# Kernel optimization log

Measured on AMD Instinct MI355X. Metric: run time of the kernel, lower is better.

## Reference

```python
import jax, jax.numpy as jnp
import numpy as np


def setup_inputs() -> dict:
    key = jax.random.key(0)
    k0, k1, k2, k3, k4 = jax.random.split(key, 5)
    B, d_inner, L, d_state = 64, 384, 197, 16
    x = jax.random.normal(k0, (B, d_inner, L), dtype=jnp.float32)
    # deltaA = exp(delta*A) lies in (0,1); uniform keeps the recurrence stable
    deltaA = jax.random.uniform(k1, (B, d_inner, L, d_state), dtype=jnp.float32)
    deltaB = jax.random.normal(k2, (B, d_inner, L, d_state), dtype=jnp.float32)
    C = jax.random.normal(k3, (B, d_state, L), dtype=jnp.float32)
    D = jax.random.normal(k4, (d_inner,), dtype=jnp.float32)
    return {"x": x, "deltaA": deltaA, "deltaB": deltaB, "C": C, "D": D}


def reference(x, deltaA, deltaB, C, D):
    """Selective scan: h_t = deltaB_t*x_t + deltaA_t*h_{t-1}; y_t = h_t @ C_t.
    x:(B,d,L) deltaA/deltaB:(B,d,L,n) C:(B,n,L) D:(d,)
    """
    deltaB_x = deltaB * x[..., None]              # (B,d,L,n)
    dA_t = jnp.moveaxis(deltaA, 2, 0)             # (L,B,d,n)
    dBx_t = jnp.moveaxis(deltaB_x, 2, 0)          # (L,B,d,n)
    C_t = jnp.moveaxis(C, 2, 0)                   # (L,B,n)

    def step(h, inputs):
        a, bx, c = inputs
        h = bx + a * h                            # (B,d,n)
        y = jnp.einsum("bdn,bn->bd", h, c)        # (B,d)
        return h, y

    h0 = jnp.zeros(dA_t.shape[1:], dtype=x.dtype)
    _, ys = jax.lax.scan(step, h0, (dA_t, dBx_t, C_t))  # ys: (L,B,d)
    y = jnp.moveaxis(ys, 0, 2)                    # (B,d,L)
    return y + x * D[:, None]
```

## Files before the change

### kernel.cpp

```cpp
#include <hip/hip_runtime.h>


#define B_   64
#define DIN  384
#define L_   197
#define N_   16
#define BUFW 2176
#define WAVEW (2*BUFW)
#define CS_OFF (2*WAVEW)
#define LDSW (CS_OFF + L_*N_)

typedef unsigned int u32as1 __attribute__((address_space(1)));
typedef unsigned int u32as3 __attribute__((address_space(3)));

__device__ __forceinline__ void gll16(const float* g, float* l) {
    __builtin_amdgcn_global_load_lds((const u32as1*)g, (u32as3*)l, 16, 0, 0);
}
__device__ __forceinline__ void gll4(const float* g, float* l) {
    __builtin_amdgcn_global_load_lds((const u32as1*)g, (u32as3*)l, 4, 0, 0);
}

template<int CTRL>
__device__ __forceinline__ float dppadd(float p) {
    return p + __int_as_float(__builtin_amdgcn_update_dpp(
        0, __float_as_int(p), CTRL, 0xF, 0xF, true));
}
__device__ __forceinline__ float sum16(float p) {
    p = dppadd<0xB1>(p);
    p = dppadd<0x4E>(p);
    p = dppadd<0x141>(p);
    p = dppadd<0x140>(p);
    return p;
}

__global__ __launch_bounds__(128)
void ssm_burst(const float* __restrict__ x, const float* __restrict__ dA,
               const float* __restrict__ dB, const float* __restrict__ C,
               const float* __restrict__ D, float* __restrict__ y)
{
    __shared__ __align__(16) float lds[LDSW];

    const int tid = threadIdx.x;
    const int b   = blockIdx.y;
    const int d0  = blockIdx.x * 8;

    const float* Cg = C + (size_t)b * (N_ * L_);
    for (int i = tid; i < N_ * L_; i += 128) {
        const int n = i / L_;
        const int t = i - n * L_;
        lds[CS_OFF + t * N_ + n] = Cg[i];
    }
    __syncthreads();

    const int wav  = tid >> 6;
    const int lane = tid & 63;
    const int g    = lane >> 4;
    const int n    = lane & 15;

    const int bd0 = b * DIN + d0 + wav * 4;
    const float* Arow = dA + (size_t)bd0 * (L_ * N_);
    const float* Brow = dB + (size_t)bd0 * (L_ * N_);
    const float* Xrow = x  + (size_t)bd0 * L_;
    float*       Yrow = y  + (size_t)(bd0 + g) * L_;
    const float  Dd   = D[d0 + wav * 4 + g];

    float* wl = lds + wav * WAVEW;
    const int lane4 = lane * 4;

#define STAGE(buf, t0) do { \
    float* _d = wl + (buf) * BUFW; \
    gll16(Arow + 0*(L_*N_) + (t0)*16 + lane4, _d + 0*264); \
    gll16(Arow + 1*(L_*N_) + (t0)*16 + lane4, _d + 1*264); \
    gll16(Arow + 2*(L_*N_) + (t0)*16 + lane4, _d + 2*264); \
    gll16(Arow + 3*(L_*N_) + (t0)*16 + lane4, _d + 3*264); \
    gll16(Brow + 0*(L_*N_) + (t0)*16 + lane4, _d + 1056 + 0*264); \
    gll16(Brow + 1*(L_*N_) + (t0)*16 + lane4, _d + 1056 + 1*264); \
    gll16(Brow + 2*(L_*N_) + (t0)*16 + lane4, _d + 1056 + 2*264); \
    gll16(Brow + 3*(L_*N_) + (t0)*16 + lane4, _d + 1056 + 3*264); \
    gll4(Xrow + g * L_ + (t0) + n, _d + 2112); \
} while (0)

#define STEP(j, xv, tg0, J0) do { \
    if ((j) >= (J0)) { \
        const float _a = _ab[g*264 + (j)*16 + n]; \
        const float _g = _ab[1056 + g*264 + (j)*16 + n]; \
        h = fmaf(_a, h, _g * (xv)); \
        float _p = h * lds[CS_OFF + ((tg0)+(j))*16 + n]; \
        _p = sum16(_p); \
        const float _yt = fmaf((xv), Dd, _p); \
        _ys = (n == (j)) ? _yt : _ys; \
    } \
} while (0)

#define TILEBODY(buf, tg0, J0) do { \
    const float* _ab = wl + (buf) * BUFW; \
    float _ys = 0.f; \
    const float4 _x0 = *(const float4*)(_ab + 2112 + g*16 + 0); \
    const float4 _x1 = *(const float4*)(_ab + 2112 + g*16 + 4); \
    const float4 _x2 = *(const float4*)(_ab + 2112 + g*16 + 8); \
    const float4 _x3 = *(const float4*)(_ab + 2112 + g*16 + 12); \
    STEP( 0, _x0.x, tg0, J0); STEP( 1, _x0.y, tg0, J0); \
    STEP( 2, _x0.z, tg0, J0); STEP( 3, _x0.w, tg0, J0); \
    STEP( 4, _x1.x, tg0, J0); STEP( 5, _x1.y, tg0, J0); \
    STEP( 6, _x1.z, tg0, J0); STEP( 7, _x1.w, tg0, J0); \
    STEP( 8, _x2.x, tg0, J0); STEP( 9, _x2.y, tg0, J0); \
    STEP(10, _x2.z, tg0, J0); STEP(11, _x2.w, tg0, J0); \
    STEP(12, _x3.x, tg0, J0); STEP(13, _x3.y, tg0, J0); \
    STEP(14, _x3.z, tg0, J0); STEP(15, _x3.w, tg0, J0); \
    if ((J0) == 0) Yrow[(tg0) + n] = _ys; \
    else if (n >= (J0)) Yrow[(tg0) + n] = _ys; \
} while (0)

    float h = 0.f;

    STAGE(0, 0);
    STAGE(1, 16);
    asm volatile("s_waitcnt vmcnt(9)" ::: "memory");
    TILEBODY(0, 0, 0);

#pragma unroll 1
    for (int k = 1; k <= 11; ++k) {
        const int tn = (k < 11) ? (k + 1) * 16 : 181;
        STAGE((k + 1) & 1, tn);
        asm volatile("s_waitcnt vmcnt(10)" ::: "memory");
        TILEBODY(k & 1, k * 16, 0);
    }
    asm volatile("s_waitcnt vmcnt(0)" ::: "memory");
    TILEBODY(0, 181, 11);

#undef TILEBODY
#undef STEP
#undef STAGE
}

extern "C" void kernel_launch(void* const* d_in, const int* in_sizes, int n_in,
                              void* d_out, int out_size, void* d_ws, size_t ws_size,
                              hipStream_t stream) {
    const float* x  = (const float*)d_in[0];
    const float* dA = (const float*)d_in[1];
    const float* dB = (const float*)d_in[2];
    const float* C  = (const float*)d_in[3];
    const float* D  = (const float*)d_in[4];
    float* yo = (float*)d_out;

    dim3 grid(DIN / 8, B_);
    dim3 block(128);
    ssm_burst<<<grid, block, 0, stream>>>(x, dA, dB, C, D, yo);
}
```

Before: 142.5 us.

## Halve scan tile length and double waves per block for deeper load overlap

Reworks the burst-load pipeline. Each tile now covers 8 timesteps instead of 16, and the block grows to four waves covering 16 channels, with launch bounds asking for three blocks per CU. Async global-to-LDS loads are packed two channel rows per 16-byte instruction, and the next stage is issued right after each tile. The C matrix is copied into LDS without a transpose. The aim is more outstanding memory traffic per CU and less LDS per wave, so this bandwidth-bound scan hides latency better. The cost is more loop iterations and more wait points per element.

```diff
diff --git a/kernel.cpp b/kernel.cpp
--- a/kernel.cpp
+++ b/kernel.cpp
@@ -5,10 +5,14 @@
 #define DIN  384
 #define L_   197
 #define N_   16
-#define BUFW 2176
+#define LN   (L_ * N_)
+#define TS   8
+#define NFT  24
+#define TT0  189
+#define BUFW 1120
 #define WAVEW (2*BUFW)
-#define CS_OFF (2*WAVEW)
-#define LDSW (CS_OFF + L_*N_)
+#define CS_OFF (4*WAVEW)
+#define LDSW (CS_OFF + LN)
 
 typedef unsigned int u32as1 __attribute__((address_space(1)));
 typedef unsigned int u32as3 __attribute__((address_space(3)));
@@ -33,8 +37,8 @@
     return p;
 }
 
-__global__ __launch_bounds__(128)
-void ssm_burst(const float* __restrict__ x, const float* __restrict__ dA,
+__global__ __launch_bounds__(256, 3)
+void ssm_dma12(const float* __restrict__ x, const float* __restrict__ dA,
                const float* __restrict__ dB, const float* __restrict__ C,
                const float* __restrict__ D, float* __restrict__ y)
 {
@@ -42,14 +46,10 @@
 
     const int tid = threadIdx.x;
     const int b   = blockIdx.y;
-    const int d0  = blockIdx.x * 8;
+    const int d0  = blockIdx.x * 16;
 
-    const float* Cg = C + (size_t)b * (N_ * L_);
-    for (int i = tid; i < N_ * L_; i += 128) {
-        const int n = i / L_;
-        const int t = i - n * L_;
-        lds[CS_OFF + t * N_ + n] = Cg[i];
-    }
+    const float* Cg = C + (size_t)b * LN;
+    for (int i = tid; i < LN; i += 256) lds[CS_OFF + i] = Cg[i];
     __syncthreads();
 
     const int wav  = tid >> 6;
@@ -57,78 +57,78 @@
     const int g    = lane >> 4;
     const int n    = lane & 15;
 
-    const int bd0 = b * DIN + d0 + wav * 4;
-    const float* Arow = dA + (size_t)bd0 * (L_ * N_);
-    const float* Brow = dB + (size_t)bd0 * (L_ * N_);
-    const float* Xrow = x  + (size_t)bd0 * L_;
-    float*       Yrow = y  + (size_t)(bd0 + g) * L_;
-    const float  Dd   = D[d0 + wav * 4 + g];
+    const int wc   = wav * 4;
+    const int bd0  = b * DIN + d0;
+
+    const float* srcA01 = dA + (size_t)(bd0 + wc + (lane >> 5)) * LN + (lane & 31) * 4;
+    const float* srcA23 = srcA01 + 2 * (size_t)LN;
+    const float* srcB01 = dB + (size_t)(bd0 + wc + (lane >> 5)) * LN + (lane & 31) * 4;
+    const float* srcB23 = srcB01 + 2 * (size_t)LN;
+    const int lm = lane < 32 ? lane : 31;
+    const float* srcX = x + (size_t)(bd0 + wc + (lm >> 3)) * L_ + (lm & 7);
 
     float* wl = lds + wav * WAVEW;
-    const int lane4 = lane * 4;
 
-#define STAGE(buf, t0) do { \
-    float* _d = wl + (buf) * BUFW; \
-    gll16(Arow + 0*(L_*N_) + (t0)*16 + lane4, _d + 0*264); \
-    gll16(Arow + 1*(L_*N_) + (t0)*16 + lane4, _d + 1*264); \
-    gll16(Arow + 2*(L_*N_) + (t0)*16 + lane4, _d + 2*264); \
-    gll16(Arow + 3*(L_*N_) + (t0)*16 + lane4, _d + 3*264); \
-    gll16(Brow + 0*(L_*N_) + (t0)*16 + lane4, _d + 1056 + 0*264); \
-    gll16(Brow + 1*(L_*N_) + (t0)*16 + lane4, _d + 1056 + 1*264); \
-    gll16(Brow + 2*(L_*N_) + (t0)*16 + lane4, _d + 1056 + 2*264); \
-    gll16(Brow + 3*(L_*N_) + (t0)*16 + lane4, _d + 1056 + 3*264); \
-    gll4(Xrow + g * L_ + (t0) + n, _d + 2112); \
+    float*       Yrow = y + (size_t)(bd0 + wc + g) * L_;
+    const float  Dd   = D[d0 + wc + g];
+    const float* CsL  = lds + CS_OFF + n * L_;
+    const int    aoff = (g >> 1) * 264 + (g & 1) * 128 + n;
+
+#define STAGE(bsel, t0) do { \
+    float* _d = wl + (bsel) * BUFW; \
+    gll16(srcA01 + (t0) * 16, _d +   0); \
+    gll16(srcA23 + (t0) * 16, _d + 264); \
+    gll16(srcB01 + (t0) * 16, _d + 528); \
+    gll16(srcB23 + (t0) * 16, _d + 792); \
+    gll4 (srcX   + (t0),      _d + 1056); \
 } while (0)
 
-#define STEP(j, xv, tg0, J0) do { \
+#define STEP(bufp, t0, j, J0) do { \
     if ((j) >= (J0)) { \
-        const float _a = _ab[g*264 + (j)*16 + n]; \
-        const float _g = _ab[1056 + g*264 + (j)*16 + n]; \
-        h = fmaf(_a, h, _g * (xv)); \
-        float _p = h * lds[CS_OFF + ((tg0)+(j))*16 + n]; \
+        const float _a  = (bufp)[aoff + (j) * 16]; \
+        const float _bb = (bufp)[528 + aoff + (j) * 16]; \
+        const float _xv = (bufp)[1056 + g * 8 + (j)]; \
+        h = fmaf(_a, h, _bb * _xv); \
+        float _p = h * CsL[(t0) + (j)]; \
         _p = sum16(_p); \
-        const float _yt = fmaf((xv), Dd, _p); \
-        _ys = (n == (j)) ? _yt : _ys; \
+        const float _yt = fmaf(_xv, Dd, _p); \
+        ys = (n == (j)) ? _yt : ys; \
     } \
 } while (0)
 
-#define TILEBODY(buf, tg0, J0) do { \
-    const float* _ab = wl + (buf) * BUFW; \
-    float _ys = 0.f; \
-    const float4 _x0 = *(const float4*)(_ab + 2112 + g*16 + 0); \
-    const float4 _x1 = *(const float4*)(_ab + 2112 + g*16 + 4); \
-    const float4 _x2 = *(const float4*)(_ab + 2112 + g*16 + 8); \
-    const float4 _x3 = *(const float4*)(_ab + 2112 + g*16 + 12); \
-    STEP( 0, _x0.x, tg0, J0); STEP( 1, _x0.y, tg0, J0); \
-    STEP( 2, _x0.z, tg0, J0); STEP( 3, _x0.w, tg0, J0); \
-    STEP( 4, _x1.x, tg0, J0); STEP( 5, _x1.y, tg0, J0); \
-    STEP( 6, _x1.z, tg0, J0); STEP( 7, _x1.w, tg0, J0); \
-    STEP( 8, _x2.x, tg0, J0); STEP( 9, _x2.y, tg0, J0); \
-    STEP(10, _x2.z, tg0, J0); STEP(11, _x2.w, tg0, J0); \
-    STEP(12, _x3.x, tg0, J0); STEP(13, _x3.y, tg0, J0); \
-    STEP(14, _x3.z, tg0, J0); STEP(15, _x3.w, tg0, J0); \
-    if ((J0) == 0) Yrow[(tg0) + n] = _ys; \
-    else if (n >= (J0)) Yrow[(tg0) + n] = _ys; \
+#define TILE(bsel, t0, J0) do { \
+    const float* _bp = wl + (bsel) * BUFW; \
+    STEP(_bp, t0, 0, J0); STEP(_bp, t0, 1, J0); \
+    STEP(_bp, t0, 2, J0); STEP(_bp, t0, 3, J0); \
+    STEP(_bp, t0, 4, J0); STEP(_bp, t0, 5, J0); \
+    STEP(_bp, t0, 6, J0); STEP(_bp, t0, 7, J0); \
 } while (0)
 
-    float h = 0.f;
+    float h = 0.f, ys = 0.f;
 
     STAGE(0, 0);
-    STAGE(1, 16);
-    asm volatile("s_waitcnt vmcnt(9)" ::: "memory");
-    TILEBODY(0, 0, 0);
+    STAGE(1, TS);
+    asm volatile("s_waitcnt vmcnt(5)" ::: "memory");
+    TILE(0, 0, 0);
+    if (n < 8) Yrow[n] = ys;
+    STAGE(0, 2 * TS);
 
 #pragma unroll 1
-    for (int k = 1; k <= 11; ++k) {
-        const int tn = (k < 11) ? (k + 1) * 16 : 181;
-        STAGE((k + 1) & 1, tn);
-        asm volatile("s_waitcnt vmcnt(10)" ::: "memory");
-        TILEBODY(k & 1, k * 16, 0);
+    for (int k = 1; k < NFT; ++k) {
+        asm volatile("s_waitcnt vmcnt(6)" ::: "memory");
+        const int t0 = k * TS;
+        TILE(k & 1, t0, 0);
+        if (n < 8) Yrow[t0 + n] = ys;
+        if (k < NFT - 1) {
+            const int tn = (k + 2 < NFT) ? (k + 2) * TS : TT0;
+            STAGE(k & 1, tn);
+        }
     }
-    asm volatile("s_waitcnt vmcnt(0)" ::: "memory");
-    TILEBODY(0, 181, 11);
+    asm volatile("s_waitcnt vmcnt(1)" ::: "memory");
+    TILE(0, TT0, 3);
+    if (n >= 3 && n < 8) Yrow[TT0 + n] = ys;
 
-#undef TILEBODY
+#undef TILE
 #undef STEP
 #undef STAGE
 }
@@ -143,7 +143,7 @@
     const float* D  = (const float*)d_in[4];
     float* yo = (float*)d_out;
 
-    dim3 grid(DIN / 8, B_);
-    dim3 block(128);
-    ssm_burst<<<grid, block, 0, stream>>>(x, dA, dB, C, D, yo);
+    dim3 grid(DIN / 16, B_);
+    dim3 block(256);
+    ssm_dma12<<<grid, block, 0, stream>>>(x, dA, dB, C, D, yo);
 }
```

New measurement: 141.3 us. About the same (-0.8%).
